# Optimization experiments

Hardware: AMD Instinct MI355X
Metric: run time of the kernel (lower is better)

The kernel has to match this reference:

```python
import jax, jax.numpy as jnp
import numpy as np

E, L, N_FEAT, N_NODES = 100000, 4, 20000, 20000
D, H = 64, 8
HD = H * D  # GRU hidden size = num_heads * out_dim
ALPHA = 0.001  # leaky relu slope


def setup_inputs() -> dict:
    key = jax.random.key(0)
    ks = jax.random.split(key, 8)
    s = 1.0 / np.sqrt(HD)
    return {
        "features": jax.random.normal(ks[0], (N_FEAT, D), jnp.float32),
        "edge_metapath_indices": jax.random.randint(ks[1], (E, L), 0, N_FEAT),
        "dst": jax.random.randint(ks[2], (E,), 0, N_NODES),
        "num_nodes": N_NODES,
        "w_ih": jax.random.uniform(ks[3], (3 * HD, D), jnp.float32, -s, s),
        "w_hh": jax.random.uniform(ks[4], (3 * HD, HD), jnp.float32, -s, s),
        "b_ih": jax.random.uniform(ks[5], (3 * HD,), jnp.float32, -s, s),
        "b_hh": jax.random.uniform(ks[6], (3 * HD,), jnp.float32, -s, s),
        "attn": jax.random.normal(ks[7], (H, D), jnp.float32) * 1.414 / np.sqrt(D),
    }


def _gru_last_hidden(x_seq, w_ih, w_hh, b_ih, b_hh):
    # x_seq: [L, E, D] -> final hidden [E, HD], torch GRU gate order (r, z, n)
    Eb = x_seq.shape[1]
    h0 = jnp.zeros((Eb, HD), x_seq.dtype)

    def step(h, x):
        gi = x @ w_ih.T + b_ih          # [E, 3*HD]
        gh = h @ w_hh.T + b_hh          # [E, 3*HD]
        ir, iz, inn = jnp.split(gi, 3, axis=-1)
        hr, hz, hn = jnp.split(gh, 3, axis=-1)
        r = jax.nn.sigmoid(ir + hr)
        z = jax.nn.sigmoid(iz + hz)
        n = jnp.tanh(inn + r * hn)
        h_new = (1.0 - z) * n + z * h
        return h_new, None

    h_last, _ = jax.lax.scan(step, h0, x_seq)
    return h_last


def reference(features, edge_metapath_indices, dst, num_nodes, w_ih, w_hh, b_ih, b_hh, attn):
    # edata: [E, L, D] gathered metapath node features
    edata = features[edge_metapath_indices]
    # GRU over metapath positions (torch permutes to seq-first)
    hidden = _gru_last_hidden(jnp.swapaxes(edata, 0, 1), w_ih, w_hh, b_ih, b_hh)  # [E, HD]
    eft = hidden.reshape(-1, H, D)                      # [E, H, D]
    # per-edge attention logits, leaky relu
    a = jax.nn.leaky_relu(jnp.einsum("ehd,hd->eh", eft, attn), ALPHA)  # [E, H]
    # edge softmax per destination node (segment softmax)
    amax = jax.ops.segment_max(a, dst, num_segments=num_nodes)         # [N, H]
    amax = jnp.where(jnp.isfinite(amax), amax, 0.0)
    a_exp = jnp.exp(a - amax[dst])
    denom = jax.ops.segment_sum(a_exp, dst, num_segments=num_nodes)    # [N, H]
    att = a_exp / jnp.maximum(denom[dst], 1e-12)                       # [E, H]
    # scatter-weighted sum of messages into destination nodes
    ft = jax.ops.segment_sum(eft * att[:, :, None], dst, num_segments=num_nodes)  # [N, H, D]
    return ft
```

## Files before the change

### kernel.cpp

```cpp
#include <hip/hip_runtime.h>
#include <cstdint>

typedef __attribute__((ext_vector_type(8))) short          bf16x8;
typedef __attribute__((ext_vector_type(8))) unsigned short u16x8;
typedef __attribute__((ext_vector_type(4))) float          f32x4;

__device__ __forceinline__ unsigned short f2bf(float x) {
    union { float f; unsigned u; } v; v.f = x;
    unsigned r = v.u + 0x7FFF + ((v.u >> 16) & 1);
    return (unsigned short)(r >> 16);
}
__device__ __forceinline__ float bf2f(unsigned short b) {
    union { float f; unsigned u; } v; v.u = ((unsigned)b) << 16;
    return v.f;
}

#define EB   64
#define NTHR 512

__global__ __launch_bounds__(256) void conv_kernel(
    const float* __restrict__ feat, const float* __restrict__ w_ih,
    const float* __restrict__ w_hh,
    unsigned short* __restrict__ featb, unsigned short* __restrict__ wbi,
    unsigned short* __restrict__ wbh, int nfeat8)
{
    int t = blockIdx.x * 256 + threadIdx.x;
    if (t < nfeat8) {
        u16x8 o;
        #pragma unroll
        for (int i = 0; i < 8; ++i) o[i] = f2bf(feat[(size_t)t * 8 + i]);
        *(u16x8*)&featb[(size_t)t * 8] = o;
    } else if (t < nfeat8 + 98304) {
        int tt = t - nfeat8;
        int lane = tt & 63, q = tt >> 6;
        int jt = q >> 4, kb = q & 15;
        int j = jt * 16 + (lane & 15);
        int k0 = kb * 32 + (lane >> 4) * 8;
        u16x8 o;
        #pragma unroll
        for (int i = 0; i < 8; ++i) o[i] = f2bf(w_hh[(size_t)j * 512 + k0 + i]);
        *(u16x8*)&wbh[(size_t)tt * 8] = o;
    } else if (t < nfeat8 + 98304 + 12288) {
        int uu = t - nfeat8 - 98304;
        int lane = uu & 63, q = uu >> 6;
        int jt = q >> 1, kb = q & 1;
        int j = jt * 16 + (lane & 15);
        int k0 = kb * 32 + (lane >> 4) * 8;
        u16x8 o;
        #pragma unroll
        for (int i = 0; i < 8; ++i) o[i] = f2bf(w_ih[(size_t)j * 64 + k0 + i]);
        *(u16x8*)&wbi[(size_t)uu * 8] = o;
    }
}

__global__ __launch_bounds__(NTHR, 2) void gru_mfma_kernel(
    const unsigned short* __restrict__ featb,
    const int* __restrict__ emi,
    const unsigned short* __restrict__ wbi,
    const unsigned short* __restrict__ wbh,
    const float* __restrict__ b_ih,
    const float* __restrict__ b_hh,
    float* __restrict__ eft,
    int E)
{
    __shared__ unsigned short hb[2][EB * 512];
    __shared__ unsigned short xb[EB * 64];

    const int tid  = threadIdx.x;
    const int lane = tid & 63;
    const int w    = tid >> 6;
    const int g    = lane >> 4;
    const int c    = lane & 15;
    const int e0   = blockIdx.x * EB;
    const f32x4 fzero = {0.f, 0.f, 0.f, 0.f};

    for (int l = 0; l < 4; ++l) {
        const int rbuf = (l + 1) & 1;
        const int wbuf = l & 1;
        {
            int r = tid >> 3, p = tid & 7;
            int nidx = (e0 + r < E) ? emi[(e0 + r) * 4 + l] : 0;
            u16x8 v = *(const u16x8*)(featb + (size_t)nidx * 64 + p * 8);
            *(u16x8*)&xb[r * 64 + ((p * 8) ^ ((r & 7) << 3))] = v;
        }
        __syncthreads();

        for (int cc = 0; cc < 4; ++cc) {
            const int j0 = (w << 6) + (cc << 4);
            const int jt = j0 >> 4;
            f32x4 ar[4], az[4], ain[4], ahn[4];
            #pragma unroll
            for (int m = 0; m < 4; ++m) { ar[m] = fzero; az[m] = fzero; ain[m] = fzero; ahn[m] = fzero; }

            {
                bf16x8 r0 = *(const bf16x8*)(wbi + (((size_t)((jt     ) * 2 + 0)) * 64 + lane) * 8);
                bf16x8 r1 = *(const bf16x8*)(wbi + (((size_t)((jt     ) * 2 + 1)) * 64 + lane) * 8);
                bf16x8 z0 = *(const bf16x8*)(wbi + (((size_t)((32 + jt) * 2 + 0)) * 64 + lane) * 8);
                bf16x8 z1 = *(const bf16x8*)(wbi + (((size_t)((32 + jt) * 2 + 1)) * 64 + lane) * 8);
                bf16x8 n0 = *(const bf16x8*)(wbi + (((size_t)((64 + jt) * 2 + 0)) * 64 + lane) * 8);
                bf16x8 n1 = *(const bf16x8*)(wbi + (((size_t)((64 + jt) * 2 + 1)) * 64 + lane) * 8);
                #pragma unroll
                for (int m = 0; m < 4; ++m) {
                    int row = m * 16 + c;
                    bf16x8 a0 = *(const bf16x8*)&xb[row * 64 + ((g * 8) ^ ((row & 7) << 3))];
                    ar[m]  = __builtin_amdgcn_mfma_f32_16x16x32_bf16(a0, r0, ar[m], 0, 0, 0);
                    az[m]  = __builtin_amdgcn_mfma_f32_16x16x32_bf16(a0, z0, az[m], 0, 0, 0);
                    ain[m] = __builtin_amdgcn_mfma_f32_16x16x32_bf16(a0, n0, ain[m], 0, 0, 0);
                    bf16x8 a1 = *(const bf16x8*)&xb[row * 64 + ((32 + g * 8) ^ ((row & 7) << 3))];
                    ar[m]  = __builtin_amdgcn_mfma_f32_16x16x32_bf16(a1, r1, ar[m], 0, 0, 0);
                    az[m]  = __builtin_amdgcn_mfma_f32_16x16x32_bf16(a1, z1, az[m], 0, 0, 0);
                    ain[m] = __builtin_amdgcn_mfma_f32_16x16x32_bf16(a1, n1, ain[m], 0, 0, 0);
                }
            }
            if (l > 0) {
                const unsigned short* hrow = &hb[rbuf][0];
                bf16x8 pr[2], pz[2], pn[2];
                pr[0] = *(const bf16x8*)(wbh + (((size_t)((jt     ) * 16 + 0)) * 64 + lane) * 8);
                pr[1] = *(const bf16x8*)(wbh + (((size_t)((jt     ) * 16 + 1)) * 64 + lane) * 8);
                pz[0] = *(const bf16x8*)(wbh + (((size_t)((32 + jt) * 16 + 0)) * 64 + lane) * 8);
                pz[1] = *(const bf16x8*)(wbh + (((size_t)((32 + jt) * 16 + 1)) * 64 + lane) * 8);
                pn[0] = *(const bf16x8*)(wbh + (((size_t)((64 + jt) * 16 + 0)) * 64 + lane) * 8);
                pn[1] = *(const bf16x8*)(wbh + (((size_t)((64 + jt) * 16 + 1)) * 64 + lane) * 8);
                #pragma unroll
                for (int kb = 0; kb < 16; ++kb) {
                    const int cur = kb & 1;
                    bf16x8 br = pr[cur], bz = pz[cur], bn = pn[cur];
                    if (kb + 2 < 16) {
                        pr[cur] = *(const bf16x8*)(wbh + (((size_t)((jt     ) * 16 + kb + 2)) * 64 + lane) * 8);
                        pz[cur] = *(const bf16x8*)(wbh + (((size_t)((32 + jt) * 16 + kb + 2)) * 64 + lane) * 8);
                        pn[cur] = *(const bf16x8*)(wbh + (((size_t)((64 + jt) * 16 + kb + 2)) * 64 + lane) * 8);
                    }
                    #pragma unroll
                    for (int m = 0; m < 4; ++m) {
                        int row = m * 16 + c;
                        bf16x8 a = *(const bf16x8*)&hrow[row * 512 + ((kb * 32 + g * 8) ^ ((row & 7) << 3))];
                        ar[m]  = __builtin_amdgcn_mfma_f32_16x16x32_bf16(a, br, ar[m], 0, 0, 0);
                        az[m]  = __builtin_amdgcn_mfma_f32_16x16x32_bf16(a, bz, az[m], 0, 0, 0);
                        ahn[m] = __builtin_amdgcn_mfma_f32_16x16x32_bf16(a, bn, ahn[m], 0, 0, 0);
                    }
                }
            }
            const int j = j0 + c;
            const float brr = b_ih[j] + b_hh[j];
            const float bzz = b_ih[512 + j] + b_hh[512 + j];
            const float bin = b_ih[1024 + j];
            const float bhn = b_hh[1024 + j];
            #pragma unroll
            for (int m = 0; m < 4; ++m) {
                #pragma unroll
                for (int q = 0; q < 4; ++q) {
                    int row = m * 16 + g * 4 + q;
                    float hold = (l > 0) ? bf2f(hb[rbuf][row * 512 + (j ^ ((row & 7) << 3))]) : 0.f;
                    float r  = 1.f / (1.f + __expf(-(ar[m][q] + brr)));
                    float z  = 1.f / (1.f + __expf(-(az[m][q] + bzz)));
                    float pn2 = ain[m][q] + bin + r * (ahn[m][q] + bhn);
                    float ex = __expf(-2.f * pn2);
                    float n  = (1.f - ex) / (1.f + ex);
                    float hnew = (1.f - z) * n + z * hold;
                    if (l < 3) {
                        hb[wbuf][row * 512 + (j ^ ((row & 7) << 3))] = f2bf(hnew);
                    } else {
                        int e = e0 + row;
                        if (e < E) eft[(size_t)e * 512 + j] = hnew;
                    }
                }
            }
        }
        __syncthreads();
    }
}

__global__ __launch_bounds__(256) void attn_kernel(
    const float* __restrict__ eft, const float* __restrict__ attn,
    const int* __restrict__ dst, float* __restrict__ aexp,
    float* __restrict__ denom, int E)
{
    int gidx = blockIdx.x * 256 + threadIdx.x;
    if (gidx >= E * 8) return;
    int e = gidx >> 3, h = gidx & 7;
    const float* fp = &eft[(size_t)e * 512 + (h << 6)];
    const float* ap = &attn[h << 6];
    float a = 0.f;
    #pragma unroll
    for (int k = 0; k < 16; ++k) {
        float4 f = *(const float4*)(fp + (k << 2));
        float4 wv = *(const float4*)(ap + (k << 2));
        a += f.x * wv.x + f.y * wv.y + f.z * wv.z + f.w * wv.w;
    }
    a = (a > 0.f) ? a : 0.001f * a;
    float ae = __expf(a);
    aexp[gidx] = ae;
    atomicAdd(&denom[(size_t)dst[e] * 8 + h], ae);
}

__global__ __launch_bounds__(256) void scatter_kernel(
    const float* __restrict__ eft, const float* __restrict__ aexp,
    const float* __restrict__ denom, const int* __restrict__ dst,
    float* __restrict__ out, long long total)
{
    long long gi = (long long)blockIdx.x * 256 + threadIdx.x;
    if (gi >= total) return;
    int e = (int)(gi >> 9);
    int j = (int)(gi & 511);
    int h = j >> 6;
    int n = dst[e];
    float wv = aexp[(size_t)e * 8 + h] / fmaxf(denom[(size_t)n * 8 + h], 1e-12f);
    atomicAdd(&out[(size_t)n * 512 + j], eft[gi] * wv);
}

extern "C" void kernel_launch(void* const* d_in, const int* in_sizes, int n_in,
                              void* d_out, int out_size, void* d_ws, size_t ws_size,
                              hipStream_t stream)
{
    const float* feat = (const float*)d_in[0];
    const int*   emi  = (const int*)d_in[1];
    const int*   dst  = (const int*)d_in[2];
    const float* w_ih = (const float*)d_in[4];
    const float* w_hh = (const float*)d_in[5];
    const float* b_ih = (const float*)d_in[6];
    const float* b_hh = (const float*)d_in[7];
    const float* attn = (const float*)d_in[8];

    const int E = in_sizes[1] / 4;
    const int N = out_size / 512;
    const int nfeat8 = in_sizes[0] / 8;

    float* eft = (float*)d_ws;
    unsigned short* featb = (unsigned short*)(eft + (size_t)E * 512);
    unsigned short* wbi   = featb + (size_t)(in_sizes[0]);
    unsigned short* wbh   = wbi + (size_t)96 * 2 * 64 * 8;
    float* aexp  = (float*)featb;
    float* denom = aexp + (size_t)E * 8;
    float* out   = (float*)d_out;

    int conv_total = nfeat8 + 98304 + 12288;
    conv_kernel<<<(conv_total + 255) / 256, 256, 0, stream>>>(
        feat, w_ih, w_hh, featb, wbi, wbh, nfeat8);

    gru_mfma_kernel<<<(E + EB - 1) / EB, NTHR, 0, stream>>>(
        featb, emi, wbi, wbh, b_ih, b_hh, eft, E);

    (void)hipMemsetAsync(denom, 0, (size_t)N * 8 * sizeof(float), stream);
    (void)hipMemsetAsync(d_out, 0, (size_t)out_size * sizeof(float), stream);

    attn_kernel<<<(E * 8 + 255) / 256, 256, 0, stream>>>(eft, attn, dst, aexp, denom, E);

    long long total = (long long)E * 512;
    scatter_kernel<<<(int)((total + 255) / 256), 256, 0, stream>>>(
        eft, aexp, denom, dst, out, total);
}
```

Before: 1.509 ms.

## Single-buffer GRU hidden state in LDS, stage new h in registers

The double-buffered hidden-state LDS array becomes a single buffer, which halves shared memory (from about 136KB to about 72KB per block). Launch bounds are raised to request four blocks per CU. New hidden values are packed into bf16 pairs and held in registers until a barrier, then written back to LDS, with the next x gather moved after that write. The weight prefetch double-buffering in the recurrent loop is dropped, which adds register pressure from the staged h values and may expose global load latency.

```diff
diff --git a/kernel.cpp b/kernel.cpp
--- a/kernel.cpp
+++ b/kernel.cpp
@@ -13,6 +13,9 @@
 __device__ __forceinline__ float bf2f(unsigned short b) {
     union { float f; unsigned u; } v; v.u = ((unsigned)b) << 16;
     return v.f;
+}
+__device__ __forceinline__ unsigned pack2bf(float a, float b) {
+    return (unsigned)f2bf(a) | ((unsigned)f2bf(b) << 16);
 }
 
 #define EB   64
@@ -53,7 +56,7 @@
     }
 }
 
-__global__ __launch_bounds__(NTHR, 2) void gru_mfma_kernel(
+__global__ __launch_bounds__(NTHR, 4) void gru_mfma_kernel(
     const unsigned short* __restrict__ featb,
     const int* __restrict__ emi,
     const unsigned short* __restrict__ wbi,
@@ -63,7 +66,7 @@
     float* __restrict__ eft,
     int E)
 {
-    __shared__ unsigned short hb[2][EB * 512];
+    __shared__ unsigned short hb[EB * 512];
     __shared__ unsigned short xb[EB * 64];
 
     const int tid  = threadIdx.x;
@@ -74,17 +77,18 @@
     const int e0   = blockIdx.x * EB;
     const f32x4 fzero = {0.f, 0.f, 0.f, 0.f};
 
+    {
+        int r = tid >> 3, p = tid & 7;
+        int nidx = (e0 + r < E) ? emi[(e0 + r) * 4 + 0] : 0;
+        u16x8 v = *(const u16x8*)(featb + (size_t)nidx * 64 + p * 8);
+        *(u16x8*)&xb[r * 64 + ((p * 8) ^ ((r & 7) << 3))] = v;
+    }
+    __syncthreads();
+
     for (int l = 0; l < 4; ++l) {
-        const int rbuf = (l + 1) & 1;
-        const int wbuf = l & 1;
-        {
-            int r = tid >> 3, p = tid & 7;
-            int nidx = (e0 + r < E) ? emi[(e0 + r) * 4 + l] : 0;
-            u16x8 v = *(const u16x8*)(featb + (size_t)nidx * 64 + p * 8);
-            *(u16x8*)&xb[r * 64 + ((p * 8) ^ ((r & 7) << 3))] = v;
-        }
-        __syncthreads();
-
+        unsigned hn[4][8];
+
+        #pragma unroll
         for (int cc = 0; cc < 4; ++cc) {
             const int j0 = (w << 6) + (cc << 4);
             const int jt = j0 >> 4;
@@ -113,27 +117,15 @@
                 }
             }
             if (l > 0) {
-                const unsigned short* hrow = &hb[rbuf][0];
-                bf16x8 pr[2], pz[2], pn[2];
-                pr[0] = *(const bf16x8*)(wbh + (((size_t)((jt     ) * 16 + 0)) * 64 + lane) * 8);
-                pr[1] = *(const bf16x8*)(wbh + (((size_t)((jt     ) * 16 + 1)) * 64 + lane) * 8);
-                pz[0] = *(const bf16x8*)(wbh + (((size_t)((32 + jt) * 16 + 0)) * 64 + lane) * 8);
-                pz[1] = *(const bf16x8*)(wbh + (((size_t)((32 + jt) * 16 + 1)) * 64 + lane) * 8);
-                pn[0] = *(const bf16x8*)(wbh + (((size_t)((64 + jt) * 16 + 0)) * 64 + lane) * 8);
-                pn[1] = *(const bf16x8*)(wbh + (((size_t)((64 + jt) * 16 + 1)) * 64 + lane) * 8);
                 #pragma unroll
                 for (int kb = 0; kb < 16; ++kb) {
-                    const int cur = kb & 1;
-                    bf16x8 br = pr[cur], bz = pz[cur], bn = pn[cur];
-                    if (kb + 2 < 16) {
-                        pr[cur] = *(const bf16x8*)(wbh + (((size_t)((jt     ) * 16 + kb + 2)) * 64 + lane) * 8);
-                        pz[cur] = *(const bf16x8*)(wbh + (((size_t)((32 + jt) * 16 + kb + 2)) * 64 + lane) * 8);
-                        pn[cur] = *(const bf16x8*)(wbh + (((size_t)((64 + jt) * 16 + kb + 2)) * 64 + lane) * 8);
-                    }
+                    bf16x8 br = *(const bf16x8*)(wbh + (((size_t)((jt     ) * 16 + kb)) * 64 + lane) * 8);
+                    bf16x8 bz = *(const bf16x8*)(wbh + (((size_t)((32 + jt) * 16 + kb)) * 64 + lane) * 8);
+                    bf16x8 bn = *(const bf16x8*)(wbh + (((size_t)((64 + jt) * 16 + kb)) * 64 + lane) * 8);
                     #pragma unroll
                     for (int m = 0; m < 4; ++m) {
                         int row = m * 16 + c;
-                        bf16x8 a = *(const bf16x8*)&hrow[row * 512 + ((kb * 32 + g * 8) ^ ((row & 7) << 3))];
+                        bf16x8 a = *(const bf16x8*)&hb[row * 512 + ((kb * 32 + g * 8) ^ ((row & 7) << 3))];
                         ar[m]  = __builtin_amdgcn_mfma_f32_16x16x32_bf16(a, br, ar[m], 0, 0, 0);
                         az[m]  = __builtin_amdgcn_mfma_f32_16x16x32_bf16(a, bz, az[m], 0, 0, 0);
                         ahn[m] = __builtin_amdgcn_mfma_f32_16x16x32_bf16(a, bn, ahn[m], 0, 0, 0);
@@ -147,26 +139,52 @@
             const float bhn = b_hh[1024 + j];
             #pragma unroll
             for (int m = 0; m < 4; ++m) {
+                float hv[4];
                 #pragma unroll
                 for (int q = 0; q < 4; ++q) {
                     int row = m * 16 + g * 4 + q;
-                    float hold = (l > 0) ? bf2f(hb[rbuf][row * 512 + (j ^ ((row & 7) << 3))]) : 0.f;
+                    float hold = (l > 0) ? bf2f(hb[row * 512 + (j ^ ((row & 7) << 3))]) : 0.f;
                     float r  = 1.f / (1.f + __expf(-(ar[m][q] + brr)));
                     float z  = 1.f / (1.f + __expf(-(az[m][q] + bzz)));
                     float pn2 = ain[m][q] + bin + r * (ahn[m][q] + bhn);
                     float ex = __expf(-2.f * pn2);
                     float n  = (1.f - ex) / (1.f + ex);
-                    float hnew = (1.f - z) * n + z * hold;
-                    if (l < 3) {
-                        hb[wbuf][row * 512 + (j ^ ((row & 7) << 3))] = f2bf(hnew);
-                    } else {
+                    hv[q] = (1.f - z) * n + z * hold;
+                    if (l == 3) {
                         int e = e0 + row;
-                        if (e < E) eft[(size_t)e * 512 + j] = hnew;
+                        if (e < E) eft[(size_t)e * 512 + j] = hv[q];
                     }
                 }
+                hn[cc][m * 2 + 0] = pack2bf(hv[0], hv[1]);
+                hn[cc][m * 2 + 1] = pack2bf(hv[2], hv[3]);
             }
         }
-        __syncthreads();
+
+        if (l < 3) {
+            __syncthreads();
+            #pragma unroll
+            for (int cc = 0; cc < 4; ++cc) {
+                const int j = (w << 6) + (cc << 4) + c;
+                #pragma unroll
+                for (int m = 0; m < 4; ++m) {
+                    #pragma unroll
+                    for (int p = 0; p < 2; ++p) {
+                        unsigned v = hn[cc][m * 2 + p];
+                        int row0 = m * 16 + g * 4 + 2 * p;
+                        int row1 = row0 + 1;
+                        hb[row0 * 512 + (j ^ ((row0 & 7) << 3))] = (unsigned short)(v & 0xFFFF);
+                        hb[row1 * 512 + (j ^ ((row1 & 7) << 3))] = (unsigned short)(v >> 16);
+                    }
+                }
+            }
+            {
+                int r = tid >> 3, p = tid & 7;
+                int nidx = (e0 + r < E) ? emi[(e0 + r) * 4 + (l + 1)] : 0;
+                u16x8 v = *(const u16x8*)(featb + (size_t)nidx * 64 + p * 8);
+                *(u16x8*)&xb[r * 64 + ((p * 8) ^ ((r & 7) << 3))] = v;
+            }
+            __syncthreads();
+        }
     }
 }
 
```

Result: slower. 3.472 ms (+130.0%).
